# Kernel optimization log

Measured on AMD Instinct MI355X. Metric: run time of the kernel, lower is better.

Reference implementation:

```python
import jax, jax.numpy as jnp
import numpy as np

B, S, D, H, T = 16, 512, 512, 8, 8
DK = D // H
SCALE = float(1.0 / np.sqrt(DK))
EPS = 1e-5


def setup_inputs() -> dict:
    key = jax.random.key(0)
    ks = jax.random.split(key, 12)
    s = float(1.0 / np.sqrt(D))  # torch Linear default init scale
    u = lambda k, shp: jax.random.uniform(k, shp, jnp.float32, -s, s)
    return {
        "x": jax.random.normal(ks[0], (B, S, D), jnp.float32),
        "x_type": jax.random.randint(ks[1], (B, S), 0, T, jnp.int32),
        "mask": jax.random.randint(ks[2], (B, S, S), 0, 2, jnp.int32),
        "Wq": u(ks[3], (T, D, D)), "bq": u(ks[4], (T, D)),
        "Wk": u(ks[5], (T, D, D)), "bk": u(ks[6], (T, D)),
        "Wv": u(ks[7], (T, D, D)), "bv": u(ks[8], (T, D)),
        "Wa": u(ks[9], (T, D, D)), "ba": u(ks[10], (T, D)),
        "gamma": jnp.ones((T, D), jnp.float32),
        "beta": jnp.zeros((T, D), jnp.float32),
    }


def _typed_proj(xf, t, W, b):
    # per-node-type linear 'experts': compute all T projections, select by type id
    # xf: [N, D], W: [T, D, D], b: [T, D], t: [N] -> [N, D]
    all_p = jnp.einsum('nd,tdh->nth', xf, W) + b[None]  # [N, T, D]
    return jnp.take_along_axis(all_p, t[:, None, None], axis=1)[:, 0]


def reference(x, x_type, mask, Wq, bq, Wk, bk, Wv, bv, Wa, ba, gamma, beta):
    xf = x.reshape(-1, D)          # [N, D], N = B*S
    t = x_type.reshape(-1)         # [N]

    # heterogeneous Q/K/V dispatch
    q = _typed_proj(xf, t, Wq, bq).reshape(B, S, H, DK).transpose(0, 2, 1, 3)
    k = _typed_proj(xf, t, Wk, bk).reshape(B, S, H, DK).transpose(0, 2, 1, 3)
    v = _typed_proj(xf, t, Wv, bv).reshape(B, S, H, DK).transpose(0, 2, 1, 3)

    # scaled dot-product attention with boolean mask (mask==0 -> -1e9)
    scores = jnp.einsum('bhqd,bhkd->bhqk', q, k) * SCALE  # [B, H, S, S]
    scores = jnp.where(mask[:, None] == 0, jnp.float32(-1e9), scores)
    p = jax.nn.softmax(scores, axis=-1)
    att = jnp.einsum('bhqk,bhkd->bhqd', p, v)             # [B, H, S, DK]
    att = att.transpose(0, 2, 1, 3).reshape(-1, D)        # [N, D]

    # per-type output projection + residual + per-type LayerNorm
    a = _typed_proj(att, t, Wa, ba)
    h = a + xf
    mu = jnp.mean(h, axis=-1, keepdims=True)
    var = jnp.mean((h - mu) ** 2, axis=-1, keepdims=True)
    out = (h - mu) * jax.lax.rsqrt(var + EPS) * gamma[t] + beta[t]
    return out.reshape(B, S, D)
```

## Files before the change

kernel.cpp:

```cpp
#include <hip/hip_runtime.h>
#include <hip/hip_bf16.h>

typedef __attribute__((ext_vector_type(8))) short short8;
typedef __attribute__((ext_vector_type(4))) float f32x4;
typedef __attribute__((ext_vector_type(4))) unsigned short u16x4;
typedef unsigned short u16;
typedef unsigned long long u64;

#define NB 16
#define NS 512
#define ND 512
#define NH 8
#define NT 8
#define NDK 64
#define NN (NB*NS)
#define SCALE_LOG2E 0.18033688011112042f
#define BM 128
#define BN 128
#define BKK 64

__device__ __forceinline__ u16 f2bf(float f) {
    __hip_bfloat16 h = __float2bfloat16(f);
    return *reinterpret_cast<u16*>(&h);
}

__global__ __launch_bounds__(256) void bucketize(
    const int* __restrict__ xty, int* __restrict__ perm, int* __restrict__ typeoff,
    int* __restrict__ tile_type, int* __restrict__ tile_row0, int* __restrict__ ntiles)
{
    __shared__ int cnt[NT], off[NT + 1], cur[NT];
    int tid = threadIdx.x;
    if (tid < NT) cnt[tid] = 0;
    __syncthreads();
    for (int n = tid; n < NN; n += 256) atomicAdd(&cnt[xty[n]], 1);
    __syncthreads();
    if (tid == 0) {
        int acc = 0, nt = 0;
        for (int t = 0; t < NT; ++t) {
            off[t] = acc;
            for (int r = 0; r < cnt[t]; r += BM) { tile_type[nt] = t; tile_row0[nt] = acc + r; ++nt; }
            acc += cnt[t];
        }
        off[NT] = acc;
        *ntiles = nt;
        for (int t = 0; t <= NT; ++t) typeoff[t] = off[t];
    }
    __syncthreads();
    if (tid < NT) cur[tid] = off[tid];
    __syncthreads();
    for (int n = tid; n < NN; n += 256) {
        int t = xty[n];
        int p = atomicAdd(&cur[t], 1);
        perm[p] = n;
    }
}

__global__ __launch_bounds__(256) void cvt_x(const float* __restrict__ x, u16* __restrict__ xb)
{
    int i = blockIdx.x * 256 + threadIdx.x;
    float4 v = reinterpret_cast<const float4*>(x)[i];
    u16x4 o;
    o.x = f2bf(v.x); o.y = f2bf(v.y); o.z = f2bf(v.z); o.w = f2bf(v.w);
    reinterpret_cast<u16x4*>(xb)[i] = o;
}

__global__ __launch_bounds__(256) void cvt_w(
    const float* __restrict__ Wq, const float* __restrict__ Wk,
    const float* __restrict__ Wv, const float* __restrict__ Wa,
    u16* __restrict__ Wqt, u16* __restrict__ Wkt, u16* __restrict__ Wvt, u16* __restrict__ Wat)
{
    int arr = blockIdx.z >> 3, t = blockIdx.z & 7;
    const float* W = (arr == 0 ? Wq : arr == 1 ? Wk : arr == 2 ? Wv : Wa) + ((size_t)t << 18);
    u16* O = (arr == 0 ? Wqt : arr == 1 ? Wkt : arr == 2 ? Wvt : Wat) + ((size_t)t << 18);
    int d0 = blockIdx.x * 64, h0 = blockIdx.y * 64;
    __shared__ __align__(16) float tile[64][68];
    int tx = threadIdx.x & 15, ty = threadIdx.x >> 4;
    #pragma unroll
    for (int i = 0; i < 4; ++i) {
        int r = ty + i * 16;
        float4 v = *reinterpret_cast<const float4*>(&W[(size_t)(d0 + r) * ND + h0 + tx * 4]);
        *reinterpret_cast<float4*>(&tile[r][tx * 4]) = v;
    }
    __syncthreads();
    #pragma unroll
    for (int i = 0; i < 4; ++i) {
        int r = ty + i * 16;
        u16x4 o;
        o.x = f2bf(tile[tx * 4 + 0][r]);
        o.y = f2bf(tile[tx * 4 + 1][r]);
        o.z = f2bf(tile[tx * 4 + 2][r]);
        o.w = f2bf(tile[tx * 4 + 3][r]);
        *reinterpret_cast<u16x4*>(&O[(size_t)(h0 + r) * ND + d0 + tx * 4]) = o;
    }
}

__global__ __launch_bounds__(256) void pack_mask(const int* __restrict__ mask, u64* __restrict__ maskb)
{
    int i = blockIdx.x * 256 + threadIdx.x;
    int v = mask[i];
    u64 bal = __ballot(v != 0);
    if ((threadIdx.x & 63) == 0) maskb[i >> 6] = bal;
}

__global__ __launch_bounds__(256) void qkv_gemm(
    const u16* __restrict__ xb,
    const u16* __restrict__ Wqt, const u16* __restrict__ Wkt, const u16* __restrict__ Wvt,
    const float* __restrict__ bq, const float* __restrict__ bk, const float* __restrict__ bv,
    const int* __restrict__ perm, const int* __restrict__ typeoff,
    const int* __restrict__ tile_type, const int* __restrict__ tile_row0, const int* __restrict__ ntiles,
    u16* __restrict__ qb, u16* __restrict__ kbf, u16* __restrict__ vtb)
{
    if (blockIdx.x >= *ntiles) return;
    int t = tile_type[blockIdx.x];
    int row0 = tile_row0[blockIdx.x];
    int rows = typeoff[t + 1] - row0; if (rows > BM) rows = BM;
    int proj = blockIdx.y >> 2;
    int col0 = (blockIdx.y & 3) * BN;
    const u16* W = (proj == 0 ? Wqt : proj == 1 ? Wkt : Wvt) + ((size_t)t << 18);
    const float* bias = (proj == 0 ? bq : proj == 1 ? bk : bv) + (t << 9);

    __shared__ __align__(16) u16 As[BM][BKK];
    __shared__ __align__(16) u16 Bs[BN][BKK];
    __shared__ int stok[BM];

    int tid = threadIdx.x;
    if (tid < BM) stok[tid] = perm[row0 + (tid < rows ? tid : 0)];
    __syncthreads();

    int lane = tid & 63, wave = tid >> 6;
    int wr = wave >> 1, wc = wave & 1;
    int fr = lane & 15, fk = (lane >> 4) << 3;

    f32x4 acc[4][4] = {};

    for (int k0 = 0; k0 < ND; k0 += BKK) {
        #pragma unroll
        for (int c = 0; c < 4; ++c) {
            int idx = c * 256 + tid;
            int r = idx >> 3, cc = (idx & 7) << 3;
            *reinterpret_cast<short8*>(&As[r][cc]) =
                *reinterpret_cast<const short8*>(xb + ((size_t)stok[r] << 9) + k0 + cc);
            *reinterpret_cast<short8*>(&Bs[r][cc]) =
                *reinterpret_cast<const short8*>(W + ((size_t)(col0 + r) << 9) + k0 + cc);
        }
        __syncthreads();
        #pragma unroll
        for (int ks = 0; ks < 2; ++ks) {
            short8 af[4], bfr[4];
            #pragma unroll
            for (int m = 0; m < 4; ++m)
                af[m] = *reinterpret_cast<const short8*>(&As[wr * 64 + m * 16 + fr][ks * 32 + fk]);
            #pragma unroll
            for (int n = 0; n < 4; ++n)
                bfr[n] = *reinterpret_cast<const short8*>(&Bs[wc * 64 + n * 16 + fr][ks * 32 + fk]);
            #pragma unroll
            for (int m = 0; m < 4; ++m)
                #pragma unroll
                for (int n = 0; n < 4; ++n)
                    acc[m][n] = __builtin_amdgcn_mfma_f32_16x16x32_bf16(af[m], bfr[n], acc[m][n], 0, 0, 0);
        }
        __syncthreads();
    }

    int rbase = (lane >> 4) << 2;
    #pragma unroll
    for (int n = 0; n < 4; ++n) {
        int c = col0 + wc * 64 + n * 16 + fr;
        float bv_ = bias[c];
        int h = c >> 6, dk = c & 63;
        #pragma unroll
        for (int m = 0; m < 4; ++m) {
            #pragma unroll
            for (int i = 0; i < 4; ++i) {
                int r = wr * 64 + m * 16 + rbase + i;
                if (r < rows) {
                    int tok = stok[r];
                    int b = tok >> 9, s = tok & 511;
                    float val = acc[m][n][i] + bv_;
                    if (proj == 0)
                        qb[((size_t)((b * NH + h) * NS + s) << 6) + dk] = f2bf(val * SCALE_LOG2E);
                    else if (proj == 1)
                        kbf[((size_t)((b * NH + h) * NS + s) << 6) + dk] = f2bf(val);
                    else
                        vtb[(size_t)((b * NH + h) * NDK + dk) * NS + s] = f2bf(val);
                }
            }
        }
    }
}

__global__ __launch_bounds__(256) void attn_mfma(
    const u16* __restrict__ qb, const u16* __restrict__ kbf, const u16* __restrict__ vtb,
    const u64* __restrict__ maskb, u16* __restrict__ attb)
{
    int bh = blockIdx.y;
    int b = bh >> 3, h = bh & 7;
    int q0 = blockIdx.x * 64;
    int tid = threadIdx.x, lane = tid & 63, w = tid >> 6;
    int ln15 = lane & 15, g = lane >> 4;

    __shared__ __align__(16) u16 sK[64 * 64];
    __shared__ __align__(16) u16 sVt[64 * 64];
    __shared__ __align__(16) u16 sP[4 * 16 * 72];

    const u16* Qg = qb + ((size_t)(bh * NS + q0 + w * 16 + ln15) << 6);
    short8 aq0 = *reinterpret_cast<const short8*>(Qg + g * 8);
    short8 aq1 = *reinterpret_cast<const short8*>(Qg + 32 + g * 8);

    const u16* Kg = kbf + ((size_t)bh << 15);
    const u16* Vtg = vtb + ((size_t)bh << 15);
    int srow = tid >> 3, schunk = tid & 7;

    const u64* Mrow = maskb + (size_t)((b << 9) + q0 + w * 16 + g * 4) * 8;

    f32x4 acc_o[4] = {};
    float mrun[4], lrun[4];
    #pragma unroll
    for (int i = 0; i < 4; ++i) { mrun[i] = -3.0e38f; lrun[i] = 0.f; }

    short8 kpre0 = *reinterpret_cast<const short8*>(Kg + ((size_t)srow << 6) + schunk * 8);
    short8 kpre1 = *reinterpret_cast<const short8*>(Kg + ((size_t)(srow + 32) << 6) + schunk * 8);
    short8 vpre0 = *reinterpret_cast<const short8*>(Vtg + (size_t)srow * NS + schunk * 8);
    short8 vpre1 = *reinterpret_cast<const short8*>(Vtg + (size_t)(srow + 32) * NS + schunk * 8);

    u16* sPw = sP + w * 16 * 72;

    for (int j = 0; j < 8; ++j) {
        __syncthreads();
        {
            int r2 = srow + 32;
            *reinterpret_cast<short8*>((char*)sK  + srow * 128 + ((schunk * 16) ^ ((srow & 7) << 4))) = kpre0;
            *reinterpret_cast<short8*>((char*)sK  + r2   * 128 + ((schunk * 16) ^ ((r2   & 7) << 4))) = kpre1;
            *reinterpret_cast<short8*>((char*)sVt + srow * 128 + ((schunk * 16) ^ ((srow & 7) << 4))) = vpre0;
            *reinterpret_cast<short8*>((char*)sVt + r2   * 128 + ((schunk * 16) ^ ((r2   & 7) << 4))) = vpre1;
        }
        if (j < 7) {
            int j1 = j + 1;
            kpre0 = *reinterpret_cast<const short8*>(Kg + ((size_t)(j1 * 64 + srow) << 6) + schunk * 8);
            kpre1 = *reinterpret_cast<const short8*>(Kg + ((size_t)(j1 * 64 + srow + 32) << 6) + schunk * 8);
            vpre0 = *reinterpret_cast<const short8*>(Vtg + (size_t)srow * NS + j1 * 64 + schunk * 8);
            vpre1 = *reinterpret_cast<const short8*>(Vtg + (size_t)(srow + 32) * NS + j1 * 64 + schunk * 8);
        }
        __syncthreads();

        f32x4 accs[4] = {};
        #pragma unroll
        for (int ks = 0; ks < 2; ++ks) {
            short8 a = ks ? aq1 : aq0;
            #pragma unroll
            for (int n = 0; n < 4; ++n) {
                int row = n * 16 + ln15;
                short8 bk = *reinterpret_cast<const short8*>(
                    (char*)sK + row * 128 + (((ks * 64) + g * 16) ^ ((row & 7) << 4)));
                accs[n] = __builtin_amdgcn_mfma_f32_16x16x32_bf16(a, bk, accs[n], 0, 0, 0);
            }
        }

        #pragma unroll
        for (int i = 0; i < 4; ++i) {
            u64 mw = Mrow[(size_t)i * 8 + j];
            float sv[4];
            #pragma unroll
            for (int n = 0; n < 4; ++n)
                sv[n] = ((mw >> (n * 16 + ln15)) & 1ull) ? accs[n][i] : -1.0e9f;
            float mx = fmaxf(fmaxf(sv[0], sv[1]), fmaxf(sv[2], sv[3]));
            #pragma unroll
            for (int d = 1; d < 16; d <<= 1) mx = fmaxf(mx, __shfl_xor(mx, d));
            float nm = fmaxf(mrun[i], mx);
            float sc = exp2f(mrun[i] - nm);
            float ps = 0.f;
            #pragma unroll
            for (int n = 0; n < 4; ++n) {
                float p = exp2f(sv[n] - nm);
                ps += p;
                sPw[(g * 4 + i) * 72 + n * 16 + ln15] = f2bf(p);
            }
            mrun[i] = nm;
            lrun[i] = lrun[i] * sc + ps;
            #pragma unroll
            for (int n2 = 0; n2 < 4; ++n2) acc_o[n2][i] *= sc;
        }

        #pragma unroll
        for (int ks = 0; ks < 2; ++ks) {
            short8 ap = *reinterpret_cast<const short8*>(
                (char*)sPw + ((ln15 * 72 + ks * 32 + g * 8) << 1));
            #pragma unroll
            for (int n2 = 0; n2 < 4; ++n2) {
                int row = n2 * 16 + ln15;
                short8 bv = *reinterpret_cast<const short8*>(
                    (char*)sVt + row * 128 + (((ks * 64) + g * 16) ^ ((row & 7) << 4)));
                acc_o[n2] = __builtin_amdgcn_mfma_f32_16x16x32_bf16(ap, bv, acc_o[n2], 0, 0, 0);
            }
        }
    }

    float linv[4];
    #pragma unroll
    for (int i = 0; i < 4; ++i) {
        float l = lrun[i];
        #pragma unroll
        for (int d = 1; d < 16; d <<= 1) l += __shfl_xor(l, d);
        linv[i] = 1.f / l;
    }
    #pragma unroll
    for (int n2 = 0; n2 < 4; ++n2) {
        #pragma unroll
        for (int i = 0; i < 4; ++i) {
            int q = q0 + w * 16 + g * 4 + i;
            attb[((size_t)((b << 9) + q) << 9) + (h << 6) + n2 * 16 + ln15] =
                f2bf(acc_o[n2][i] * linv[i]);
        }
    }
}

__global__ __launch_bounds__(256) void out_gemm(
    const u16* __restrict__ attb, const u16* __restrict__ Wat, const float* __restrict__ ba,
    const int* __restrict__ perm, const int* __restrict__ typeoff,
    const int* __restrict__ tile_type, const int* __restrict__ tile_row0, const int* __restrict__ ntiles,
    const float* __restrict__ x, float* __restrict__ hbuf)
{
    if (blockIdx.x >= *ntiles) return;
    int t = tile_type[blockIdx.x];
    int row0 = tile_row0[blockIdx.x];
    int rows = typeoff[t + 1] - row0; if (rows > BM) rows = BM;
    int col0 = blockIdx.y * BN;
    const u16* W = Wat + ((size_t)t << 18);
    const float* bias = ba + (t << 9);

    __shared__ __align__(16) u16 As[BM][BKK];
    __shared__ __align__(16) u16 Bs[BN][BKK];
    __shared__ int stok[BM];

    int tid = threadIdx.x;
    if (tid < BM) stok[tid] = perm[row0 + (tid < rows ? tid : 0)];
    __syncthreads();

    int lane = tid & 63, wave = tid >> 6;
    int wr = wave >> 1, wc = wave & 1;
    int fr = lane & 15, fk = (lane >> 4) << 3;

    f32x4 acc[4][4] = {};

    for (int k0 = 0; k0 < ND; k0 += BKK) {
        #pragma unroll
        for (int c = 0; c < 4; ++c) {
            int idx = c * 256 + tid;
            int r = idx >> 3, cc = (idx & 7) << 3;
            *reinterpret_cast<short8*>(&As[r][cc]) =
                *reinterpret_cast<const short8*>(attb + ((size_t)stok[r] << 9) + k0 + cc);
            *reinterpret_cast<short8*>(&Bs[r][cc]) =
                *reinterpret_cast<const short8*>(W + ((size_t)(col0 + r) << 9) + k0 + cc);
        }
        __syncthreads();
        #pragma unroll
        for (int ks = 0; ks < 2; ++ks) {
            short8 af[4], bfr[4];
            #pragma unroll
            for (int m = 0; m < 4; ++m)
                af[m] = *reinterpret_cast<const short8*>(&As[wr * 64 + m * 16 + fr][ks * 32 + fk]);
            #pragma unroll
            for (int n = 0; n < 4; ++n)
                bfr[n] = *reinterpret_cast<const short8*>(&Bs[wc * 64 + n * 16 + fr][ks * 32 + fk]);
            #pragma unroll
            for (int m = 0; m < 4; ++m)
                #pragma unroll
                for (int n = 0; n < 4; ++n)
                    acc[m][n] = __builtin_amdgcn_mfma_f32_16x16x32_bf16(af[m], bfr[n], acc[m][n], 0, 0, 0);
        }
        __syncthreads();
    }

    int rbase = (lane >> 4) << 2;
    #pragma unroll
    for (int n = 0; n < 4; ++n) {
        int c = col0 + wc * 64 + n * 16 + fr;
        float bv_ = bias[c];
        #pragma unroll
        for (int m = 0; m < 4; ++m) {
            #pragma unroll
            for (int i = 0; i < 4; ++i) {
                int r = wr * 64 + m * 16 + rbase + i;
                if (r < rows) {
                    int tok = stok[r];
                    size_t off = (size_t)tok * ND + c;
                    hbuf[off] = acc[m][n][i] + bv_ + x[off];
                }
            }
        }
    }
}

__global__ __launch_bounds__(256) void lnorm(
    const float* __restrict__ hbuf, const int* __restrict__ xty,
    const float* __restrict__ gamma, const float* __restrict__ beta, float* __restrict__ out)
{
    int row = blockIdx.x * 4 + (threadIdx.x >> 6);
    int lane = threadIdx.x & 63;
    const float4* h4 = reinterpret_cast<const float4*>(hbuf + (size_t)row * ND);
    float4 a = h4[lane * 2], b = h4[lane * 2 + 1];
    float sum = a.x + a.y + a.z + a.w + b.x + b.y + b.z + b.w;
    float sq = a.x * a.x + a.y * a.y + a.z * a.z + a.w * a.w
             + b.x * b.x + b.y * b.y + b.z * b.z + b.w * b.w;
    #pragma unroll
    for (int off = 32; off; off >>= 1) { sum += __shfl_xor(sum, off); sq += __shfl_xor(sq, off); }
    float mu = sum * (1.f / ND);
    float var = sq * (1.f / ND) - mu * mu;
    float is = rsqrtf(var + 1e-5f);
    int t = xty[row];
    const float4* g4 = reinterpret_cast<const float4*>(gamma + ((size_t)t << 9));
    const float4* be4 = reinterpret_cast<const float4*>(beta + ((size_t)t << 9));
    float4 g0 = g4[lane * 2], g1 = g4[lane * 2 + 1];
    float4 b0 = be4[lane * 2], b1 = be4[lane * 2 + 1];
    float4 o0, o1;
    o0.x = (a.x - mu) * is * g0.x + b0.x;
    o0.y = (a.y - mu) * is * g0.y + b0.y;
    o0.z = (a.z - mu) * is * g0.z + b0.z;
    o0.w = (a.w - mu) * is * g0.w + b0.w;
    o1.x = (b.x - mu) * is * g1.x + b1.x;
    o1.y = (b.y - mu) * is * g1.y + b1.y;
    o1.z = (b.z - mu) * is * g1.z + b1.z;
    o1.w = (b.w - mu) * is * g1.w + b1.w;
    float4* out4 = reinterpret_cast<float4*>(out + (size_t)row * ND);
    out4[lane * 2] = o0; out4[lane * 2 + 1] = o1;
}

extern "C" void kernel_launch(void* const* d_in, const int* in_sizes, int n_in,
                              void* d_out, int out_size, void* d_ws, size_t ws_size,
                              hipStream_t stream)
{
    const float* x     = (const float*)d_in[0];
    const int*   xty   = (const int*)d_in[1];
    const int*   mask  = (const int*)d_in[2];
    const float* Wq    = (const float*)d_in[3];
    const float* bq    = (const float*)d_in[4];
    const float* Wk    = (const float*)d_in[5];
    const float* bk    = (const float*)d_in[6];
    const float* Wv    = (const float*)d_in[7];
    const float* bv    = (const float*)d_in[8];
    const float* Wa    = (const float*)d_in[9];
    const float* ba    = (const float*)d_in[10];
    const float* gamma = (const float*)d_in[11];
    const float* beta  = (const float*)d_in[12];
    float* out = (float*)d_out;

    char* ws = (char*)d_ws;
    u16*   xb      = (u16*)(ws + 0);
    u16*   Wqt     = (u16*)(ws + 8388608);
    u16*   Wkt     = (u16*)(ws + 12582912);
    u16*   Wvt     = (u16*)(ws + 16777216);
    u16*   Wat     = (u16*)(ws + 20971520);
    u16*   qb      = (u16*)(ws + 25165824);
    u16*   kbf     = (u16*)(ws + 33554432);
    u16*   vtb     = (u16*)(ws + 41943040);
    u16*   attb    = (u16*)(ws + 50331648);
    float* hbuf    = (float*)(ws + 58720256);
    u64*   maskb   = (u64*)(ws + 75497472);
    int*   perm    = (int*)(ws + 76021760);
    int*   typeoff = (int*)(ws + 76054528);
    int*   ttile   = (int*)(ws + 76054592);
    int*   trow    = (int*)(ws + 76054912);
    int*   ntiles  = (int*)(ws + 76055232);

    bucketize<<<dim3(1), dim3(256), 0, stream>>>(xty, perm, typeoff, ttile, trow, ntiles);
    cvt_x<<<dim3(4096), dim3(256), 0, stream>>>(x, xb);
    cvt_w<<<dim3(8, 8, 32), dim3(256), 0, stream>>>(Wq, Wk, Wv, Wa, Wqt, Wkt, Wvt, Wat);
    pack_mask<<<dim3(16384), dim3(256), 0, stream>>>(mask, maskb);
    qkv_gemm<<<dim3(72, 12), dim3(256), 0, stream>>>(xb, Wqt, Wkt, Wvt, bq, bk, bv,
                                                     perm, typeoff, ttile, trow, ntiles, qb, kbf, vtb);
    attn_mfma<<<dim3(8, 128), dim3(256), 0, stream>>>(qb, kbf, vtb, maskb, attb);
    out_gemm<<<dim3(72, 4), dim3(256), 0, stream>>>(attb, Wat, ba,
                                                    perm, typeoff, ttile, trow, ntiles, x, hbuf);
    lnorm<<<dim3(2048), dim3(256), 0, stream>>>(hbuf, xty, gamma, beta, out);
}
```

Baseline: 299.3 us.

## Use direct global-to-LDS loads with XOR swizzle in GEMMs; transpose V separately

Both typed GEMMs now stage A and B tiles with global_load_lds 16-byte direct-to-LDS loads, using an XOR-swizzled chunk layout. This is meant to cut register round-trips and LDS bank conflicts on the fragment reads, and the loop's sync placement is reordered to match. The QKV epilogue writes V in the same row-major layout as Q and K instead of doing strided transposed scalar stores. A new transp_v kernel then builds the transposed V through shared memory. This adds one launch and an extra V buffer pass in exchange for coalesced stores.

```diff
diff --git a/kernel.cpp b/kernel.cpp
--- a/kernel.cpp
+++ b/kernel.cpp
@@ -24,6 +24,13 @@
     return *reinterpret_cast<u16*>(&h);
 }
 
+typedef const __attribute__((address_space(1))) void* gas_t;
+typedef __attribute__((address_space(3))) void* las_t;
+
+__device__ __forceinline__ void gload16(const void* gsrc, void* ldst) {
+    __builtin_amdgcn_global_load_lds((gas_t)gsrc, (las_t)ldst, 16, 0, 0);
+}
+
 __global__ __launch_bounds__(256) void bucketize(
     const int* __restrict__ xty, int* __restrict__ perm, int* __restrict__ typeoff,
     int* __restrict__ tile_type, int* __restrict__ tile_row0, int* __restrict__ ntiles)
@@ -108,7 +115,7 @@
     const float* __restrict__ bq, const float* __restrict__ bk, const float* __restrict__ bv,
     const int* __restrict__ perm, const int* __restrict__ typeoff,
     const int* __restrict__ tile_type, const int* __restrict__ tile_row0, const int* __restrict__ ntiles,
-    u16* __restrict__ qb, u16* __restrict__ kbf, u16* __restrict__ vtb)
+    u16* __restrict__ qb, u16* __restrict__ kbf, u16* __restrict__ vb)
 {
     if (blockIdx.x >= *ntiles) return;
     int t = tile_type[blockIdx.x];
@@ -118,6 +125,8 @@
     int col0 = (blockIdx.y & 3) * BN;
     const u16* W = (proj == 0 ? Wqt : proj == 1 ? Wkt : Wvt) + ((size_t)t << 18);
     const float* bias = (proj == 0 ? bq : proj == 1 ? bk : bv) + (t << 9);
+    u16* outp = proj == 0 ? qb : proj == 1 ? kbf : vb;
+    float qscale = proj == 0 ? SCALE_LOG2E : 1.f;
 
     __shared__ __align__(16) u16 As[BM][BKK];
     __shared__ __align__(16) u16 Bs[BN][BKK];
@@ -127,42 +136,52 @@
     if (tid < BM) stok[tid] = perm[row0 + (tid < rows ? tid : 0)];
     __syncthreads();
 
-    int lane = tid & 63, wave = tid >> 6;
-    int wr = wave >> 1, wc = wave & 1;
-    int fr = lane & 15, fk = (lane >> 4) << 3;
+    int lane = tid & 63, w = tid >> 6;
+    int wr = w >> 1, wc = w & 1;
+    int fr = lane & 15, g = lane >> 4;
+
+    int lrow = lane >> 3;
+    int schunk = (lane & 7) ^ lrow;
+    int tokA[4];
+    #pragma unroll
+    for (int k = 0; k < 4; ++k) tokA[k] = stok[w * 32 + k * 8 + lrow];
 
     f32x4 acc[4][4] = {};
 
     for (int k0 = 0; k0 < ND; k0 += BKK) {
-        #pragma unroll
-        for (int c = 0; c < 4; ++c) {
-            int idx = c * 256 + tid;
-            int r = idx >> 3, cc = (idx & 7) << 3;
-            *reinterpret_cast<short8*>(&As[r][cc]) =
-                *reinterpret_cast<const short8*>(xb + ((size_t)stok[r] << 9) + k0 + cc);
-            *reinterpret_cast<short8*>(&Bs[r][cc]) =
-                *reinterpret_cast<const short8*>(W + ((size_t)(col0 + r) << 9) + k0 + cc);
-        }
         __syncthreads();
+        #pragma unroll
+        for (int k = 0; k < 4; ++k) {
+            gload16(xb + (((size_t)tokA[k]) << 9) + k0 + schunk * 8, &As[w * 32 + k * 8][0]);
+            gload16(W + (((size_t)(col0 + w * 32 + k * 8 + lrow)) << 9) + k0 + schunk * 8,
+                    &Bs[w * 32 + k * 8][0]);
+        }
+        __syncthreads();
+
+        const char* Ab = (const char*)As;
+        const char* Bb = (const char*)Bs;
         #pragma unroll
         for (int ks = 0; ks < 2; ++ks) {
             short8 af[4], bfr[4];
             #pragma unroll
-            for (int m = 0; m < 4; ++m)
-                af[m] = *reinterpret_cast<const short8*>(&As[wr * 64 + m * 16 + fr][ks * 32 + fk]);
-            #pragma unroll
-            for (int n = 0; n < 4; ++n)
-                bfr[n] = *reinterpret_cast<const short8*>(&Bs[wc * 64 + n * 16 + fr][ks * 32 + fk]);
+            for (int m = 0; m < 4; ++m) {
+                int r = wr * 64 + m * 16 + fr;
+                af[m] = *reinterpret_cast<const short8*>(Ab + r * 128 + (((ks * 4 + g) ^ (r & 7)) << 4));
+            }
+            #pragma unroll
+            for (int n = 0; n < 4; ++n) {
+                int r = wc * 64 + n * 16 + fr;
+                bfr[n] = *reinterpret_cast<const short8*>(Bb + r * 128 + (((ks * 4 + g) ^ (r & 7)) << 4));
+            }
             #pragma unroll
             for (int m = 0; m < 4; ++m)
                 #pragma unroll
                 for (int n = 0; n < 4; ++n)
                     acc[m][n] = __builtin_amdgcn_mfma_f32_16x16x32_bf16(af[m], bfr[n], acc[m][n], 0, 0, 0);
         }
-        __syncthreads();
-    }
-
-    int rbase = (lane >> 4) << 2;
+    }
+
+    int rbase = g << 2;
     #pragma unroll
     for (int n = 0; n < 4; ++n) {
         int c = col0 + wc * 64 + n * 16 + fr;
@@ -176,16 +195,36 @@
                 if (r < rows) {
                     int tok = stok[r];
                     int b = tok >> 9, s = tok & 511;
-                    float val = acc[m][n][i] + bv_;
-                    if (proj == 0)
-                        qb[((size_t)((b * NH + h) * NS + s) << 6) + dk] = f2bf(val * SCALE_LOG2E);
-                    else if (proj == 1)
-                        kbf[((size_t)((b * NH + h) * NS + s) << 6) + dk] = f2bf(val);
-                    else
-                        vtb[(size_t)((b * NH + h) * NDK + dk) * NS + s] = f2bf(val);
+                    outp[((size_t)((b * NH + h) * NS + s) << 6) + dk] =
+                        f2bf((acc[m][n][i] + bv_) * qscale);
                 }
             }
         }
+    }
+}
+
+__global__ __launch_bounds__(256) void transp_v(const u16* __restrict__ vb, u16* __restrict__ vtb)
+{
+    int bh = blockIdx.y, s0 = blockIdx.x * 64;
+    __shared__ __align__(16) u16 t[64][72];
+    int tid = threadIdx.x;
+    const u16* src = vb + ((size_t)bh << 15) + ((size_t)s0 << 6);
+    #pragma unroll
+    for (int it = 0; it < 2; ++it) {
+        int idx = it * 256 + tid;
+        int s = idx & 63, c = idx >> 6;
+        short8 v = *reinterpret_cast<const short8*>(src + ((size_t)s << 6) + c * 8);
+        #pragma unroll
+        for (int j = 0; j < 8; ++j) t[c * 8 + j][s] = ((const u16*)&v)[j];
+    }
+    __syncthreads();
+    u16* dst = vtb + ((size_t)bh << 15) + s0;
+    #pragma unroll
+    for (int it = 0; it < 2; ++it) {
+        int idx = it * 256 + tid;
+        int dk = idx >> 3, c = idx & 7;
+        short8 v = *reinterpret_cast<const short8*>(&t[dk][c * 8]);
+        *reinterpret_cast<short8*>(dst + (size_t)dk * NS + c * 8) = v;
     }
 }
 
@@ -336,42 +375,52 @@
     if (tid < BM) stok[tid] = perm[row0 + (tid < rows ? tid : 0)];
     __syncthreads();
 
-    int lane = tid & 63, wave = tid >> 6;
-    int wr = wave >> 1, wc = wave & 1;
-    int fr = lane & 15, fk = (lane >> 4) << 3;
+    int lane = tid & 63, w = tid >> 6;
+    int wr = w >> 1, wc = w & 1;
+    int fr = lane & 15, g = lane >> 4;
+
+    int lrow = lane >> 3;
+    int schunk = (lane & 7) ^ lrow;
+    int tokA[4];
+    #pragma unroll
+    for (int k = 0; k < 4; ++k) tokA[k] = stok[w * 32 + k * 8 + lrow];
 
     f32x4 acc[4][4] = {};
 
     for (int k0 = 0; k0 < ND; k0 += BKK) {
-        #pragma unroll
-        for (int c = 0; c < 4; ++c) {
-            int idx = c * 256 + tid;
-            int r = idx >> 3, cc = (idx & 7) << 3;
-            *reinterpret_cast<short8*>(&As[r][cc]) =
-                *reinterpret_cast<const short8*>(attb + ((size_t)stok[r] << 9) + k0 + cc);
-            *reinterpret_cast<short8*>(&Bs[r][cc]) =
-                *reinterpret_cast<const short8*>(W + ((size_t)(col0 + r) << 9) + k0 + cc);
-        }
         __syncthreads();
+        #pragma unroll
+        for (int k = 0; k < 4; ++k) {
+            gload16(attb + (((size_t)tokA[k]) << 9) + k0 + schunk * 8, &As[w * 32 + k * 8][0]);
+            gload16(W + (((size_t)(col0 + w * 32 + k * 8 + lrow)) << 9) + k0 + schunk * 8,
+                    &Bs[w * 32 + k * 8][0]);
+        }
+        __syncthreads();
+
+        const char* Ab = (const char*)As;
+        const char* Bb = (const char*)Bs;
         #pragma unroll
         for (int ks = 0; ks < 2; ++ks) {
             short8 af[4], bfr[4];
             #pragma unroll
-            for (int m = 0; m < 4; ++m)
-                af[m] = *reinterpret_cast<const short8*>(&As[wr * 64 + m * 16 + fr][ks * 32 + fk]);
-            #pragma unroll
-            for (int n = 0; n < 4; ++n)
-                bfr[n] = *reinterpret_cast<const short8*>(&Bs[wc * 64 + n * 16 + fr][ks * 32 + fk]);
+            for (int m = 0; m < 4; ++m) {
+                int r = wr * 64 + m * 16 + fr;
+                af[m] = *reinterpret_cast<const short8*>(Ab + r * 128 + (((ks * 4 + g) ^ (r & 7)) << 4));
+            }
+            #pragma unroll
+            for (int n = 0; n < 4; ++n) {
+                int r = wc * 64 + n * 16 + fr;
+                bfr[n] = *reinterpret_cast<const short8*>(Bb + r * 128 + (((ks * 4 + g) ^ (r & 7)) << 4));
+            }
             #pragma unroll
             for (int m = 0; m < 4; ++m)
                 #pragma unroll
                 for (int n = 0; n < 4; ++n)
                     acc[m][n] = __builtin_amdgcn_mfma_f32_16x16x32_bf16(af[m], bfr[n], acc[m][n], 0, 0, 0);
         }
-        __syncthreads();
-    }
-
-    int rbase = (lane >> 4) << 2;
+    }
+
+    int rbase = g << 2;
     #pragma unroll
     for (int n = 0; n < 4; ++n) {
         int c = col0 + wc * 64 + n * 16 + fr;
@@ -452,22 +501,24 @@
     u16*   Wat     = (u16*)(ws + 20971520);
     u16*   qb      = (u16*)(ws + 25165824);
     u16*   kbf     = (u16*)(ws + 33554432);
-    u16*   vtb     = (u16*)(ws + 41943040);
-    u16*   attb    = (u16*)(ws + 50331648);
-    float* hbuf    = (float*)(ws + 58720256);
-    u64*   maskb   = (u64*)(ws + 75497472);
-    int*   perm    = (int*)(ws + 76021760);
-    int*   typeoff = (int*)(ws + 76054528);
-    int*   ttile   = (int*)(ws + 76054592);
-    int*   trow    = (int*)(ws + 76054912);
-    int*   ntiles  = (int*)(ws + 76055232);
+    u16*   vb      = (u16*)(ws + 41943040);
+    u16*   vtb     = (u16*)(ws + 50331648);
+    u16*   attb    = (u16*)(ws + 58720256);
+    float* hbuf    = (float*)(ws + 67108864);
+    u64*   maskb   = (u64*)(ws + 83886080);
+    int*   perm    = (int*)(ws + 84410368);
+    int*   typeoff = (int*)(ws + 84443136);
+    int*   ttile   = (int*)(ws + 84443200);
+    int*   trow    = (int*)(ws + 84443520);
+    int*   ntiles  = (int*)(ws + 84443840);
 
     bucketize<<<dim3(1), dim3(256), 0, stream>>>(xty, perm, typeoff, ttile, trow, ntiles);
     cvt_x<<<dim3(4096), dim3(256), 0, stream>>>(x, xb);
     cvt_w<<<dim3(8, 8, 32), dim3(256), 0, stream>>>(Wq, Wk, Wv, Wa, Wqt, Wkt, Wvt, Wat);
     pack_mask<<<dim3(16384), dim3(256), 0, stream>>>(mask, maskb);
     qkv_gemm<<<dim3(72, 12), dim3(256), 0, stream>>>(xb, Wqt, Wkt, Wvt, bq, bk, bv,
-                                                     perm, typeoff, ttile, trow, ntiles, qb, kbf, vtb);
+                                                     perm, typeoff, ttile, trow, ntiles, qb, kbf, vb);
+    transp_v<<<dim3(8, 128), dim3(256), 0, stream>>>(vb, vtb);
     attn_mfma<<<dim3(8, 128), dim3(256), 0, stream>>>(qb, kbf, vtb, maskb, attb);
     out_gemm<<<dim3(72, 4), dim3(256), 0, stream>>>(attb, Wat, ba,
                                                     perm, typeoff, ttile, trow, ntiles, x, hbuf);
```

Result: faster. 279.3 us (-6.7%).
